# Kernel tuning notes

Hardware: AMD Instinct MI355X
Metric: run time of the kernel (lower is better)

The kernel has to match this reference:

```python
import jax, jax.numpy as jnp
import numpy as np

GROUP_SIZE = 128
IN_FEATURES = 4096
OUT_FEATURES = 11008
BATCH = 16


def setup_inputs() -> dict:
    key = jax.random.key(0)
    k_x, k_q, k_s, k_z, k_b = jax.random.split(key, 5)
    num_groups = IN_FEATURES // GROUP_SIZE
    x = jax.random.normal(k_x, (BATCH, IN_FEATURES), dtype=jnp.float32)
    # packed int4 pairs stored as bytes in [0, 256)
    qweight = jax.random.randint(k_q, (OUT_FEATURES, IN_FEATURES // 2), 0, 256, dtype=jnp.int32)
    # positive scales of realistic magnitude, zeros in [0, 15]
    scales = jax.random.uniform(k_s, (OUT_FEATURES, num_groups), dtype=jnp.float32) * 0.01 + 1e-4
    zeros = jax.random.uniform(k_z, (OUT_FEATURES, num_groups), dtype=jnp.float32) * 15.0
    bias = jax.random.normal(k_b, (OUT_FEATURES,), dtype=jnp.float32)
    return {"x": x, "qweight": qweight, "scales": scales, "zeros": zeros, "bias": bias}


def _unpack_int4(packed, in_features):
    # packed: [O, I//2] ints in [0,256); low nibble is even column, high nibble odd
    low = packed & 15
    high = (packed >> 4) & 15
    return jnp.stack([low, high], axis=-1).reshape(packed.shape[0], in_features)  # [O, I]


def reference(x, qweight, scales, zeros, bias):
    q = _unpack_int4(qweight, IN_FEATURES).astype(jnp.float32)        # [O, I]
    s = jnp.repeat(scales, GROUP_SIZE, axis=1)                        # [O, I]
    z = jnp.repeat(zeros, GROUP_SIZE, axis=1)                         # [O, I]
    w = (q - z) * s                                                   # dequantized weight [O, I]
    return x @ w.T + bias                                             # [B, O]
```

## Files before the change

### kernel.cpp

```cpp
#include <hip/hip_runtime.h>
#include <hip/hip_fp16.h>

#define IN_F   4096
#define OUT_F  11008
#define BATCH  16
#define GROUPS 32
#define PACKED_PER_ROW (IN_F / 2)

typedef __attribute__((ext_vector_type(8))) _Float16 half8;
typedef __attribute__((ext_vector_type(4))) _Float16 half4;
typedef __attribute__((ext_vector_type(2))) _Float16 h2;
typedef __attribute__((ext_vector_type(4))) float    float4_t;
typedef __attribute__((ext_vector_type(4))) int      int4_t;
typedef __attribute__((ext_vector_type(4))) unsigned uint4_t;

__device__ inline h2 cvt2(float a, float b) {
    return __builtin_bit_cast(h2, __builtin_amdgcn_cvt_pkrtz(a, b));
}

__global__ __launch_bounds__(256) void xcvt(const float* __restrict__ x,
                                            _Float16* __restrict__ xh) {
    const int i = (blockIdx.x * 256 + threadIdx.x) * 4;
    const float4_t v = *(const float4_t*)(x + i);
    half2_t_unused: ;
    half4 h;
    h2 lo = cvt2(v.x, v.y), hi = cvt2(v.z, v.w);
    h[0] = lo[0]; h[1] = lo[1]; h[2] = hi[0]; h[3] = hi[1];
    *(half4*)(xh + i) = h;
}

template<int S, bool XH>
__global__ __launch_bounds__(256) void gptq_gemm(
    const float* __restrict__ x, const _Float16* __restrict__ xh,
    const int* __restrict__ qw,
    const float* __restrict__ scales, const float* __restrict__ zeros,
    const float* __restrict__ bias, float* __restrict__ out,
    float* __restrict__ ws_part)
{
    const int tid  = threadIdx.x;
    const int lane = tid & 63;
    const int wave = tid >> 6;
    const int otile = blockIdx.x / S;
    const int ks    = blockIdx.x % S;

    const int ln = lane & 15;
    const int lk = lane >> 4;

    const int o = otile * 16 + ln;

    constexpr int KCB = IN_F / S;
    constexpr int KCW = KCB / 4;
    constexpr int NCH = KCW / 256;
    const int kc0 = ks * KCB + wave * KCW;

    const int* qbase = qw + o * PACKED_PER_ROW + (kc0 >> 1) + lk * 4;
    const float* srow = scales + o * GROUPS;
    const float* zrow = zeros  + o * GROUPS;

    float4_t acc = {0.f, 0.f, 0.f, 0.f};
    const h2 k1024 = { (_Float16)1024.0f, (_Float16)1024.0f };

    #pragma unroll
    for (int ch = 0; ch < NCH; ++ch) {
        const int cc = kc0 + ch * 256;
        h2 s2[2], c2[2];
        #pragma unroll
        for (int gi = 0; gi < 2; ++gi) {
            const int g = (cc >> 7) + gi;
            const float s  = srow[g];
            const float c0 = -zrow[g] * s;
            const _Float16 sh = (_Float16)s, chh = (_Float16)c0;
            s2[gi][0] = sh; s2[gi][1] = sh;
            c2[gi][0] = chh; c2[gi][1] = chh;
        }

        int4_t qv[8];
        #pragma unroll
        for (int t = 0; t < 8; ++t)
            qv[t] = *(const int4_t*)(qbase + ch * 128 + t * 16);

        half8 xv[8];
        #pragma unroll
        for (int t = 0; t < 8; ++t) {
            if (XH) {
                xv[t] = *(const half8*)(xh + ln * IN_F + cc + t * 32 + lk * 8);
            } else {
                const float* xp = x + ln * IN_F + cc + t * 32 + lk * 8;
                const float4_t a0 = *(const float4_t*)(xp);
                const float4_t a1 = *(const float4_t*)(xp + 4);
                h2 p0 = cvt2(a0.x, a0.y), p1 = cvt2(a0.z, a0.w);
                h2 p2 = cvt2(a1.x, a1.y), p3 = cvt2(a1.z, a1.w);
                xv[t][0]=p0[0]; xv[t][1]=p0[1]; xv[t][2]=p1[0]; xv[t][3]=p1[1];
                xv[t][4]=p2[0]; xv[t][5]=p2[1]; xv[t][6]=p3[0]; xv[t][7]=p3[1];
            }
        }

        #pragma unroll
        for (int t = 0; t < 8; ++t) {
            const int gi = t >> 2;
            uint4_t bw;
            #pragma unroll
            for (int i = 0; i < 4; ++i) {
                const unsigned pv = (unsigned)qv[t][i];
                const unsigned u = (pv & 0xFu) | ((pv << 12) & 0xF0000u)
                                 | 0x64006400u;
                h2 q = __builtin_bit_cast(h2, u) - k1024;
                h2 w = q * s2[gi] + c2[gi];
                bw[i] = __builtin_bit_cast(unsigned, w);
            }
            const half8 bf = __builtin_bit_cast(half8, bw);
            acc = __builtin_amdgcn_mfma_f32_16x16x32_f16(xv[t], bf, acc, 0, 0, 0);
        }
    }

    __shared__ float red[4][16][17];
    #pragma unroll
    for (int r = 0; r < 4; ++r) red[wave][lk * 4 + r][ln] = acc[r];
    __syncthreads();

    const int row = tid >> 4;
    const int col = tid & 15;
    const float sum = red[0][row][col] + red[1][row][col]
                    + red[2][row][col] + red[3][row][col];
    const int oo = otile * 16 + col;
    if (S == 1) {
        out[row * OUT_F + oo] = sum + bias[oo];
    } else {
        ws_part[(ks * BATCH + row) * OUT_F + oo] = sum;
    }
}

__global__ __launch_bounds__(256) void gptq_reduce(
    const float* __restrict__ ws_part, const float* __restrict__ bias,
    float* __restrict__ out, int S)
{
    const int idx = blockIdx.x * 256 + threadIdx.x;
    if (idx >= BATCH * OUT_F) return;
    const int o = idx % OUT_F;
    float sum = bias[o];
    for (int ks = 0; ks < S; ++ks)
        sum += ws_part[ks * (BATCH * OUT_F) + idx];
    out[idx] = sum;
}

extern "C" void kernel_launch(void* const* d_in, const int* in_sizes, int n_in,
                              void* d_out, int out_size, void* d_ws, size_t ws_size,
                              hipStream_t stream) {
    const float* x      = (const float*)d_in[0];
    const int*   qwgt   = (const int*)d_in[1];
    const float* scales = (const float*)d_in[2];
    const float* zeros  = (const float*)d_in[3];
    const float* bias   = (const float*)d_in[4];
    float* out = (float*)d_out;

    const int nOTiles = OUT_F / 16;
    const size_t need = (size_t)8 << 20;

    if (d_ws && ws_size >= need) {
        float*    ws_part = (float*)d_ws;
        _Float16* xh      = (_Float16*)((char*)d_ws + (4 << 20));
        constexpr int S = 4;
        hipLaunchKernelGGL(xcvt, dim3(BATCH * IN_F / 1024), dim3(256), 0, stream,
                           x, xh);
        hipLaunchKernelGGL((gptq_gemm<S, true>), dim3(nOTiles * S), dim3(256),
                           0, stream, x, xh, qwgt, scales, zeros, bias, out,
                           ws_part);
        hipLaunchKernelGGL(gptq_reduce, dim3((BATCH * OUT_F + 255) / 256),
                           dim3(256), 0, stream, ws_part, bias, out, S);
    } else {
        hipLaunchKernelGGL((gptq_gemm<1, false>), dim3(nOTiles), dim3(256),
                           0, stream, x, (const _Float16*)nullptr, qwgt,
                           scales, zeros, bias, out, (float*)nullptr);
    }
}
```

Baseline: 36.25 us.

## Use single-wave blocks with double-buffered register prefetch for int4 GEMM

The split-K GEMM moves from 256-thread blocks with four waves and an LDS reduction to 64-thread single-wave blocks. Each block handles a quarter of K and writes its partials straight to the workspace, and the reduce kernel sums those partials. Weight and activation loads are double-buffered in registers so the next chunk's loads are in flight while the current chunk is dequantized and fed to MFMA. Scales and zeros are loaded as vectors up front. This costs more blocks (2752 one-wave blocks) and higher register pressure from holding two buffers.

```diff
diff --git a/kernel.cpp b/kernel.cpp
--- a/kernel.cpp
+++ b/kernel.cpp
@@ -22,125 +22,168 @@
                                             _Float16* __restrict__ xh) {
     const int i = (blockIdx.x * 256 + threadIdx.x) * 4;
     const float4_t v = *(const float4_t*)(x + i);
-    half2_t_unused: ;
     half4 h;
     h2 lo = cvt2(v.x, v.y), hi = cvt2(v.z, v.w);
     h[0] = lo[0]; h[1] = lo[1]; h[2] = hi[0]; h[3] = hi[1];
     *(half4*)(xh + i) = h;
 }
 
-template<int S, bool XH>
-__global__ __launch_bounds__(256) void gptq_gemm(
-    const float* __restrict__ x, const _Float16* __restrict__ xh,
-    const int* __restrict__ qw,
+__global__ __launch_bounds__(64) void gptq_gemm_w(
+    const _Float16* __restrict__ xh, const int* __restrict__ qw,
     const float* __restrict__ scales, const float* __restrict__ zeros,
-    const float* __restrict__ bias, float* __restrict__ out,
     float* __restrict__ ws_part)
 {
-    const int tid  = threadIdx.x;
-    const int lane = tid & 63;
-    const int wave = tid >> 6;
-    const int otile = blockIdx.x / S;
-    const int ks    = blockIdx.x % S;
+    const int lane  = threadIdx.x;
+    const int otile = blockIdx.x >> 2;
+    const int kq    = blockIdx.x & 3;
 
     const int ln = lane & 15;
     const int lk = lane >> 4;
-
-    const int o = otile * 16 + ln;
-
-    constexpr int KCB = IN_F / S;
-    constexpr int KCW = KCB / 4;
-    constexpr int NCH = KCW / 256;
-    const int kc0 = ks * KCB + wave * KCW;
-
-    const int* qbase = qw + o * PACKED_PER_ROW + (kc0 >> 1) + lk * 4;
-    const float* srow = scales + o * GROUPS;
-    const float* zrow = zeros  + o * GROUPS;
+    const int o  = otile * 16 + ln;
+
+    const int*      qbase = qw + o * PACKED_PER_ROW + kq * 512 + lk * 4;
+    const _Float16* xbase = xh + ln * IN_F + kq * 1024 + lk * 8;
+
+    const float4_t sf0 = *(const float4_t*)(scales + o * GROUPS + kq * 8);
+    const float4_t sf1 = *(const float4_t*)(scales + o * GROUPS + kq * 8 + 4);
+    const float4_t zf0 = *(const float4_t*)(zeros  + o * GROUPS + kq * 8);
+    const float4_t zf1 = *(const float4_t*)(zeros  + o * GROUPS + kq * 8 + 4);
+    const float sArr[8] = { sf0.x, sf0.y, sf0.z, sf0.w, sf1.x, sf1.y, sf1.z, sf1.w };
+    const float zArr[8] = { zf0.x, zf0.y, zf0.z, zf0.w, zf1.x, zf1.y, zf1.z, zf1.w };
+
+    int4_t qv[2][8];
+    half8  xv[2][8];
+
+    #pragma unroll
+    for (int t = 0; t < 8; ++t) {
+        qv[0][t] = *(const int4_t*)(qbase + t * 16);
+        xv[0][t] = *(const half8*)(xbase + t * 32);
+    }
 
     float4_t acc = {0.f, 0.f, 0.f, 0.f};
     const h2 k1024 = { (_Float16)1024.0f, (_Float16)1024.0f };
 
     #pragma unroll
-    for (int ch = 0; ch < NCH; ++ch) {
-        const int cc = kc0 + ch * 256;
+    for (int c = 0; c < 4; ++c) {
+        const int cur = c & 1, nxt = cur ^ 1;
+        if (c < 3) {
+            #pragma unroll
+            for (int t = 0; t < 8; ++t) {
+                qv[nxt][t] = *(const int4_t*)(qbase + (c + 1) * 128 + t * 16);
+                xv[nxt][t] = *(const half8*)(xbase + (c + 1) * 256 + t * 32);
+            }
+        }
         h2 s2[2], c2[2];
         #pragma unroll
         for (int gi = 0; gi < 2; ++gi) {
-            const int g = (cc >> 7) + gi;
-            const float s  = srow[g];
-            const float c0 = -zrow[g] * s;
-            const _Float16 sh = (_Float16)s, chh = (_Float16)c0;
-            s2[gi][0] = sh; s2[gi][1] = sh;
-            c2[gi][0] = chh; c2[gi][1] = chh;
-        }
-
-        int4_t qv[8];
-        #pragma unroll
-        for (int t = 0; t < 8; ++t)
-            qv[t] = *(const int4_t*)(qbase + ch * 128 + t * 16);
-
-        half8 xv[8];
-        #pragma unroll
-        for (int t = 0; t < 8; ++t) {
-            if (XH) {
-                xv[t] = *(const half8*)(xh + ln * IN_F + cc + t * 32 + lk * 8);
-            } else {
-                const float* xp = x + ln * IN_F + cc + t * 32 + lk * 8;
-                const float4_t a0 = *(const float4_t*)(xp);
-                const float4_t a1 = *(const float4_t*)(xp + 4);
-                h2 p0 = cvt2(a0.x, a0.y), p1 = cvt2(a0.z, a0.w);
-                h2 p2 = cvt2(a1.x, a1.y), p3 = cvt2(a1.z, a1.w);
-                xv[t][0]=p0[0]; xv[t][1]=p0[1]; xv[t][2]=p1[0]; xv[t][3]=p1[1];
-                xv[t][4]=p2[0]; xv[t][5]=p2[1]; xv[t][6]=p3[0]; xv[t][7]=p3[1];
-            }
-        }
-
+            const float s  = sArr[2 * c + gi];
+            const float c0 = -zArr[2 * c + gi] * s;
+            s2[gi] = cvt2(s, s);
+            c2[gi] = cvt2(c0, c0);
+        }
         #pragma unroll
         for (int t = 0; t < 8; ++t) {
             const int gi = t >> 2;
             uint4_t bw;
             #pragma unroll
             for (int i = 0; i < 4; ++i) {
-                const unsigned pv = (unsigned)qv[t][i];
+                const unsigned pv = (unsigned)qv[cur][t][i];
                 const unsigned u = (pv & 0xFu) | ((pv << 12) & 0xF0000u)
                                  | 0x64006400u;
                 h2 q = __builtin_bit_cast(h2, u) - k1024;
                 h2 w = q * s2[gi] + c2[gi];
                 bw[i] = __builtin_bit_cast(unsigned, w);
             }
-            const half8 bf = __builtin_bit_cast(half8, bw);
-            acc = __builtin_amdgcn_mfma_f32_16x16x32_f16(xv[t], bf, acc, 0, 0, 0);
-        }
-    }
-
-    __shared__ float red[4][16][17];
-    #pragma unroll
-    for (int r = 0; r < 4; ++r) red[wave][lk * 4 + r][ln] = acc[r];
-    __syncthreads();
-
-    const int row = tid >> 4;
-    const int col = tid & 15;
-    const float sum = red[0][row][col] + red[1][row][col]
-                    + red[2][row][col] + red[3][row][col];
-    const int oo = otile * 16 + col;
-    if (S == 1) {
-        out[row * OUT_F + oo] = sum + bias[oo];
-    } else {
-        ws_part[(ks * BATCH + row) * OUT_F + oo] = sum;
-    }
+            acc = __builtin_amdgcn_mfma_f32_16x16x32_f16(
+                xv[cur][t], __builtin_bit_cast(half8, bw), acc, 0, 0, 0);
+        }
+    }
+
+    #pragma unroll
+    for (int r = 0; r < 4; ++r)
+        ws_part[(kq * BATCH + lk * 4 + r) * OUT_F + otile * 16 + ln] = acc[r];
 }
 
 __global__ __launch_bounds__(256) void gptq_reduce(
     const float* __restrict__ ws_part, const float* __restrict__ bias,
-    float* __restrict__ out, int S)
+    float* __restrict__ out)
 {
     const int idx = blockIdx.x * 256 + threadIdx.x;
     if (idx >= BATCH * OUT_F) return;
     const int o = idx % OUT_F;
-    float sum = bias[o];
-    for (int ks = 0; ks < S; ++ks)
-        sum += ws_part[ks * (BATCH * OUT_F) + idx];
-    out[idx] = sum;
+    out[idx] = bias[o]
+             + ws_part[idx]
+             + ws_part[1 * (BATCH * OUT_F) + idx]
+             + ws_part[2 * (BATCH * OUT_F) + idx]
+             + ws_part[3 * (BATCH * OUT_F) + idx];
+}
+
+__global__ __launch_bounds__(256) void gptq_gemm_fb(
+    const float* __restrict__ x, const int* __restrict__ qw,
+    const float* __restrict__ scales, const float* __restrict__ zeros,
+    const float* __restrict__ bias, float* __restrict__ out)
+{
+    const int tid  = threadIdx.x;
+    const int lane = tid & 63;
+    const int wave = tid >> 6;
+    const int otile = blockIdx.x;
+    const int ln = lane & 15, lk = lane >> 4;
+    const int o = otile * 16 + ln;
+    const int kc0 = wave * 1024;
+
+    const int* qbase = qw + o * PACKED_PER_ROW + (kc0 >> 1) + lk * 4;
+    const float* srow = scales + o * GROUPS;
+    const float* zrow = zeros  + o * GROUPS;
+
+    float4_t acc = {0.f, 0.f, 0.f, 0.f};
+    const h2 k1024 = { (_Float16)1024.0f, (_Float16)1024.0f };
+
+    #pragma unroll
+    for (int ch = 0; ch < 4; ++ch) {
+        const int cc = kc0 + ch * 256;
+        h2 s2[2], c2[2];
+        #pragma unroll
+        for (int gi = 0; gi < 2; ++gi) {
+            const float s  = srow[(cc >> 7) + gi];
+            const float c0 = -zrow[(cc >> 7) + gi] * s;
+            s2[gi] = cvt2(s, s); c2[gi] = cvt2(c0, c0);
+        }
+        #pragma unroll
+        for (int t = 0; t < 8; ++t) {
+            const int4_t v = *(const int4_t*)(qbase + ch * 128 + t * 16);
+            const float* xp = x + ln * IN_F + cc + t * 32 + lk * 8;
+            const float4_t a0 = *(const float4_t*)(xp);
+            const float4_t a1 = *(const float4_t*)(xp + 4);
+            half8 af;
+            h2 p0 = cvt2(a0.x, a0.y), p1 = cvt2(a0.z, a0.w);
+            h2 p2 = cvt2(a1.x, a1.y), p3 = cvt2(a1.z, a1.w);
+            af[0]=p0[0]; af[1]=p0[1]; af[2]=p1[0]; af[3]=p1[1];
+            af[4]=p2[0]; af[5]=p2[1]; af[6]=p3[0]; af[7]=p3[1];
+            const int gi = t >> 2;
+            uint4_t bw;
+            #pragma unroll
+            for (int i = 0; i < 4; ++i) {
+                const unsigned pv = (unsigned)v[i];
+                const unsigned u = (pv & 0xFu) | ((pv << 12) & 0xF0000u)
+                                 | 0x64006400u;
+                h2 q = __builtin_bit_cast(h2, u) - k1024;
+                h2 w = q * s2[gi] + c2[gi];
+                bw[i] = __builtin_bit_cast(unsigned, w);
+            }
+            acc = __builtin_amdgcn_mfma_f32_16x16x32_f16(
+                af, __builtin_bit_cast(half8, bw), acc, 0, 0, 0);
+        }
+    }
+
+    __shared__ float red[4][16][17];
+    #pragma unroll
+    for (int r = 0; r < 4; ++r) red[wave][lk * 4 + r][ln] = acc[r];
+    __syncthreads();
+    const int row = tid >> 4, col = tid & 15;
+    const float sum = red[0][row][col] + red[1][row][col]
+                    + red[2][row][col] + red[3][row][col];
+    const int oo = otile * 16 + col;
+    out[row * OUT_F + oo] = sum + bias[oo];
 }
 
 extern "C" void kernel_launch(void* const* d_in, const int* in_sizes, int n_in,
@@ -159,17 +202,14 @@
     if (d_ws && ws_size >= need) {
         float*    ws_part = (float*)d_ws;
         _Float16* xh      = (_Float16*)((char*)d_ws + (4 << 20));
-        constexpr int S = 4;
         hipLaunchKernelGGL(xcvt, dim3(BATCH * IN_F / 1024), dim3(256), 0, stream,
                            x, xh);
-        hipLaunchKernelGGL((gptq_gemm<S, true>), dim3(nOTiles * S), dim3(256),
-                           0, stream, x, xh, qwgt, scales, zeros, bias, out,
-                           ws_part);
+        hipLaunchKernelGGL(gptq_gemm_w, dim3(nOTiles * 4), dim3(64), 0, stream,
+                           xh, qwgt, scales, zeros, ws_part);
         hipLaunchKernelGGL(gptq_reduce, dim3((BATCH * OUT_F + 255) / 256),
-                           dim3(256), 0, stream, ws_part, bias, out, S);
+                           dim3(256), 0, stream, ws_part, bias, out);
     } else {
-        hipLaunchKernelGGL((gptq_gemm<1, false>), dim3(nOTiles), dim3(256),
-                           0, stream, x, (const _Float16*)nullptr, qwgt,
-                           scales, zeros, bias, out, (float*)nullptr);
-    }
-}
+        hipLaunchKernelGGL(gptq_gemm_fb, dim3(nOTiles), dim3(256), 0, stream,
+                           x, qwgt, scales, zeros, bias, out);
+    }
+}
```

Result: faster. 35.30 us (-2.6%).
